# Kernel optimization log

Hardware: AMD Instinct MI355X
Metric: run time of the kernel (lower is better)

## Reference

```python
import jax, jax.numpy as jnp
import numpy as np

N = 1024
H = 4096
W = 4096
K_COUNTS = 10
IOU_T = 0.5
NEG = -1e30  # -inf stand-in for unrecorded groups


def _box_iou(b):
    # b: [N,4] xyxy pixel coords -> [N,N] IoU (torchvision.ops.box_iou)
    area = (b[:, 2] - b[:, 0]) * (b[:, 3] - b[:, 1])
    ix1 = jnp.maximum(b[:, None, 0], b[None, :, 0])
    iy1 = jnp.maximum(b[:, None, 1], b[None, :, 1])
    ix2 = jnp.minimum(b[:, None, 2], b[None, :, 2])
    iy2 = jnp.minimum(b[:, None, 3], b[None, :, 3])
    inter = jnp.clip(ix2 - ix1, 0.0) * jnp.clip(iy2 - iy1, 0.0)
    return inter / (area[:, None] + area[None, :] - inter)


def _c_wsl(iou_gt, scores, counts):
    # Faithful vectorized c_wsl_fast: for every start box i, greedily sweep
    # j = i+1..N-1 adding boxes compatible (IoU <= T) with all current members;
    # when a group hits `counts` at the TOP of a j-iteration it is recorded
    # (check-before-add semantics, so a group completed at j = N-1 is never
    # recorded, matching the original break-based control flow). The final
    # answer is the LAST start achieving the max recorded score (>= update).
    n = scores.shape[0]
    starts = jnp.arange(n)
    carry0 = (
        jnp.eye(n, dtype=bool),            # sel[i, k]: box k in group of start i
        jnp.ones(n, jnp.int32),            # group sizes
        scores,                            # group scores
        jnp.zeros(n, bool),                # recorded flag (== break)
        jnp.full(n, NEG, scores.dtype),    # recorded score
        jnp.zeros((n, n), bool),           # recorded membership
    )

    def step(c, xs):
        j, sj, iou_j = xs  # iou_j = iou_gt[j] (> T bool row; matrix symmetric)
        sel, size, score, rec, rec_score, rec_sel = c
        active = (j > starts) & (~rec)
        do_rec = active & (size == counts)
        rec_sel = jnp.where(do_rec[:, None], sel, rec_sel)
        rec_score = jnp.where(do_rec, score, rec_score)
        rec = rec | do_rec
        compat = ~jnp.any(sel & iou_j[None, :], axis=1)
        add = active & (~do_rec) & (size < counts) & compat
        sel = sel.at[:, j].set(sel[:, j] | add)
        size = size + add.astype(size.dtype)
        score = score + jnp.where(add, sj, jnp.zeros((), score.dtype))
        return (sel, size, score, rec, rec_score, rec_sel), None

    (_, _, _, rec, rec_score, rec_sel), _ = jax.lax.scan(
        step, carry0, (starts, scores, iou_gt))
    masked = jnp.where(rec, rec_score, NEG)
    best = (n - 1) - jnp.argmax(masked[::-1])  # last argmax == '>=' update rule
    return jnp.where(jnp.any(rec), rec_sel[best], jnp.zeros(n, bool))


def reference(bbox, obj_scores, probs, counts):
    Hh, Ww = probs.shape
    # score_bbox_heatmap(reduction='mean'): mean of probs[y1:y2, x1:x2] per box,
    # computed exactly for all boxes with a zero-padded summed-area table.
    sat = jnp.pad(jnp.cumsum(jnp.cumsum(probs, axis=0), axis=1), ((1, 0), (1, 0)))
    x1 = jnp.clip(jnp.floor(bbox[:, 0]).astype(jnp.int32), 0, Ww)
    y1 = jnp.clip(jnp.floor(bbox[:, 1]).astype(jnp.int32), 0, Hh)
    x2 = jnp.clip(jnp.floor(bbox[:, 2]).astype(jnp.int32), 0, Ww)
    y2 = jnp.clip(jnp.floor(bbox[:, 3]).astype(jnp.int32), 0, Hh)
    sums = sat[y2, x2] - sat[y1, x2] - sat[y2, x1] + sat[y1, x1]
    cnt = jnp.maximum((y2 - y1) * (x2 - x1), 1).astype(probs.dtype)
    box_scores = sums / cnt
    # agg_score_method == 'mean'
    scores = 0.5 * (obj_scores + box_scores)
    # sort descending, then greedy IoU grouping on sorted boxes
    order = jnp.argsort(-scores)
    bbox_s = bbox[order]
    scores_s = scores[order]
    iou_gt = _box_iou(bbox_s) > IOU_T
    sel = _c_wsl(iou_gt, scores_s, counts)
    return scores_s * sel.astype(scores_s.dtype)


def setup_inputs() -> dict:
    key = jax.random.key(0)
    k1, k2, k3, k4, k5, k6 = jax.random.split(key, 6)
    cx = jax.random.uniform(k1, (N,), minval=0.15, maxval=0.85) * W
    cy = jax.random.uniform(k2, (N,), minval=0.15, maxval=0.85) * H
    bw = jnp.maximum(jax.random.uniform(k3, (N,), minval=0.02, maxval=0.25) * W, 8.0)
    bh = jnp.maximum(jax.random.uniform(k4, (N,), minval=0.02, maxval=0.25) * H, 8.0)
    bbox = jnp.stack([cx - bw / 2, cy - bh / 2, cx + bw / 2, cy + bh / 2], axis=1)
    obj_scores = jax.random.uniform(k5, (N,))
    probs = jax.random.uniform(k6, (H, W))
    return {"bbox": bbox, "obj_scores": obj_scores, "probs": probs, "counts": K_COUNTS}
```

## Files before the change

kernel.cpp:

```cpp
#include <hip/hip_runtime.h>

#define HH 4096
#define WW 4096
#define NB 1024
#define NCHUNK 64
#define CROWS 64
#define IOU_T 0.5f

typedef unsigned long long u64;

constexpr size_t OFF_COORDS = 0;
constexpr size_t OFF_RD     = OFF_COORDS + (size_t)NB * 16;
constexpr size_t OFF_PART   = OFF_RD     + (size_t)HH * 16;
constexpr size_t OFF_SC64   = OFF_PART   + (size_t)NCHUNK * WW * 8;
constexpr size_t OFF_ORDER  = OFF_SC64   + (size_t)NB * 8;
constexpr size_t OFF_CTR    = OFF_ORDER  + (size_t)NB * 4;
constexpr size_t OFF_IOU    = OFF_CTR    + 64;
constexpr size_t OFF_RECSC  = OFF_IOU    + (size_t)NB * 16 * 8;
constexpr size_t OFF_RECSEL = OFF_RECSC  + (size_t)NB * 8;
constexpr size_t OFF_CC     = OFF_RECSEL + (size_t)NB * 16 * 8;


__global__ void __launch_bounds__(1024) k_setup(const float* __restrict__ bbox,
                        int4* coords, int4* rowdesc, int* ctr) {
    __shared__ int lf[HH];
    __shared__ int xlo[HH];
    __shared__ int xhi[HH];
    __shared__ int psum[256];
    int t = threadIdx.x;
    if (t == 0) *ctr = 0;
    for (int k = t; k < HH; k += 1024) { lf[k] = 0; xlo[k] = WW; xhi[k] = 0; }
    __syncthreads();
    if (t < NB) {
        int i = t;
        float b0 = bbox[i * 4 + 0], b1 = bbox[i * 4 + 1];
        float b2 = bbox[i * 4 + 2], b3 = bbox[i * 4 + 3];
        int x1 = min(max((int)floorf(b0), 0), WW);
        int y1 = min(max((int)floorf(b1), 0), HH);
        int x2 = min(max((int)floorf(b2), 0), WW);
        int y2 = min(max((int)floorf(b3), 0), HH);
        coords[i] = make_int4(x1, y1, x2, y2);
        if (y1 >= 1) {
            lf[y1 - 1] = 1;
            atomicMin(&xlo[y1 - 1], x1);
            atomicMax(&xhi[y1 - 1], x2);
        }
        if (y2 >= 1) {
            lf[y2 - 1] = 1;
            atomicMin(&xlo[y2 - 1], x1);
            atomicMax(&xhi[y2 - 1], x2);
        }
    }
    __syncthreads();
    if (t < 256) {
        int base = t * 16;
        int s = 0;
        for (int k = 0; k < 16; k++) s += lf[base + k];
        psum[t] = s;
    }
    __syncthreads();
    if (t < 64) {
        int v0 = psum[t * 4], v1 = psum[t * 4 + 1];
        int v2 = psum[t * 4 + 2], v3 = psum[t * 4 + 3];
        int lsum = v0 + v1 + v2 + v3;
        int incs = lsum;
        #pragma unroll
        for (int off = 1; off < 64; off <<= 1) {
            int n = __shfl_up(incs, off);
            if (t >= off) incs += n;
        }
        int ex = incs - lsum;
        psum[t * 4]     = ex;
        psum[t * 4 + 1] = ex + v0;
        psum[t * 4 + 2] = ex + v0 + v1;
        psum[t * 4 + 3] = ex + v0 + v1 + v2;
    }
    __syncthreads();
    if (t < 256) {
        int base = t * 16;
        int run = psum[t];
        for (int k = 0; k < 16; k++) {
            int r = base + k;
            int fl = lf[r];
            rowdesc[r] = make_int4(fl ? run : -1, xlo[r] >> 2, (xhi[r] + 3) >> 2, 0);
            run += fl;
        }
    }
}

__global__ void __launch_bounds__(256) k_stage(const float* __restrict__ probs,
        const int4* __restrict__ rowdesc,
        double* __restrict__ part, float* __restrict__ Cc) {
    __shared__ int4 rd_s[CROWS];
    int tid = blockIdx.x * 256 + threadIdx.x;
    int c  = tid >> 10;
    int xq = tid & 1023;
    if (threadIdx.x < CROWS) rd_s[threadIdx.x] = rowdesc[c * CROWS + threadIdx.x];
    __syncthreads();
    const float4* p = (const float4*)probs + (size_t)c * CROWS * (WW / 4) + xq;
    float4* Cc4 = (float4*)Cc;
    double a0 = 0.0, a1 = 0.0, a2 = 0.0, a3 = 0.0;
    for (int r = 0; r < CROWS; r += 8) {
        float4 q[8];
        #pragma unroll
        for (int k = 0; k < 8; k++) q[k] = p[(size_t)(r + k) * (WW / 4)];
        #pragma unroll
        for (int k = 0; k < 8; k++) {
            a0 += (double)q[k].x; a1 += (double)q[k].y;
            a2 += (double)q[k].z; a3 += (double)q[k].w;
            int4 d = rd_s[r + k];
            if (d.x >= 0 && xq >= d.y && xq < d.z)
                Cc4[(size_t)d.x * (WW / 4) + xq] =
                    make_float4((float)a0, (float)a1, (float)a2, (float)a3);
        }
    }
    double2* pp = (double2*)(part + (size_t)c * WW) + xq * 2;
    pp[0] = make_double2(a0, a1);
    pp[1] = make_double2(a2, a3);
}

__global__ void k_chunkscan(double* __restrict__ part) {
    int x = blockIdx.x * blockDim.x + threadIdx.x;
    double carry = 0.0;
    for (int g = 0; g < NCHUNK / 16; g++) {
        double v[16];
        #pragma unroll
        for (int k = 0; k < 16; k++) v[k] = part[(size_t)(g * 16 + k) * WW + x];
        #pragma unroll
        for (int k = 0; k < 16; k++) { double tv = v[k]; v[k] = carry; carry += tv; }
        #pragma unroll
        for (int k = 0; k < 16; k++) part[(size_t)(g * 16 + k) * WW + x] = v[k];
    }
}

__global__ void __launch_bounds__(64) k_boxsum(const int4* __restrict__ coords,
                         const float* __restrict__ obj,
                         const int4* __restrict__ rowdesc, const float* __restrict__ Cc,
                         const double* __restrict__ part,
                         double* sc64) {
    int i = blockIdx.x;
    int lane = threadIdx.x;
    int4 cd = coords[i];
    bool h1 = (cd.y >= 1), h2 = (cd.w >= 1);
    int s1 = h1 ? rowdesc[cd.y - 1].x : 0;
    int s2 = h2 ? rowdesc[cd.w - 1].x : 0;
    const float*  r2 = Cc   + (size_t)(h2 ? s2 : 0) * WW;
    const double* q2 = part + (size_t)(h2 ? ((cd.w - 1) >> 6) : 0) * WW;
    const float*  r1 = Cc   + (size_t)(h1 ? s1 : 0) * WW;
    const double* q1 = part + (size_t)(h1 ? ((cd.y - 1) >> 6) : 0) * WW;
    double s = 0.0;
    for (int x = cd.x + lane; x < cd.z; x += 64) {
        double v2 = h2 ? ((double)r2[x] + q2[x]) : 0.0;
        double v1 = h1 ? ((double)r1[x] + q1[x]) : 0.0;
        s += (v2 - v1);
    }
    #pragma unroll
    for (int off = 32; off > 0; off >>= 1) s += __shfl_down(s, off);
    if (lane == 0) {
        long long cnt = (long long)(cd.w - cd.y) * (long long)(cd.z - cd.x);
        if (cnt < 1) cnt = 1;
        double box = s / (double)cnt;
        sc64[i] = 0.5 * ((double)obj[i] + box);
    }
}

__global__ void __launch_bounds__(128) k_rank(const double* __restrict__ sc64,
                                              int* __restrict__ order) {
    __shared__ double s[NB];
    int t = threadIdx.x;
    for (int k = t; k < NB; k += 128) s[k] = sc64[k];
    __syncthreads();
    int i = blockIdx.x * 128 + t;
    double si = s[i];
    int rank = 0;
    #pragma unroll 8
    for (int j = 0; j < NB; j++) {
        double sj = s[j];
        rank += (sj > si) || (sj == si && j < i);
    }
    order[rank] = i;
}

__global__ void k_iou(const int* __restrict__ order, const float* __restrict__ bbox,
                      u64* __restrict__ ioub) {
    int tid = blockIdx.x * blockDim.x + threadIdx.x;
    int i = tid >> 10;
    int j = tid & (NB - 1);
    float4 a = ((const float4*)bbox)[order[i]];
    float4 b = ((const float4*)bbox)[order[j]];
    float ai = (a.z - a.x) * (a.w - a.y);
    float aj = (b.z - b.x) * (b.w - b.y);
    float ix1 = fmaxf(a.x, b.x), iy1 = fmaxf(a.y, b.y);
    float ix2 = fminf(a.z, b.z), iy2 = fminf(a.w, b.w);
    float iw = fmaxf(ix2 - ix1, 0.0f), ih = fmaxf(iy2 - iy1, 0.0f);
    float inter = iw * ih;
    float iou_v = inter / (ai + aj - inter);
    bool bit = iou_v > IOU_T;
    u64 m = __ballot(bit);
    if ((threadIdx.x & 63) == 0) ioub[(size_t)i * 16 + (j >> 6)] = m;
}

__global__ void __launch_bounds__(64) k_group(const u64* __restrict__ ioub,
                        const int* __restrict__ order,
                        const double* __restrict__ sc64,
                        const int* __restrict__ counts,
                        double* __restrict__ recsc,
                        u64* __restrict__ recsel,
                        int* __restrict__ ctr,
                        float* __restrict__ out) {
    __shared__ double ssd_s[NB];
    __shared__ int lastflag;
    int t = threadIdx.x;
    int i = blockIdx.x * 64 + t;
    for (int k = t; k < NB; k += 64) ssd_s[k] = sc64[order[k]];
    __syncthreads();
    int K = counts[0];
    u64 inc[16], sel[16];
    int wi = i >> 6, bi = i & 63;
    #pragma unroll
    for (int w = 0; w < 16; w++) {
        inc[w] = ioub[(size_t)i * 16 + w];
        sel[w] = (w == wi) ? (1ULL << bi) : 0ULL;
    }
    int size = 1;
    double score = ssd_s[i];
    int last = i;
    #pragma unroll
    for (int w = 0; w < 16; w++) {
        if (w < wi || size >= K) continue;
        u64 avail = ~inc[w];
        if (w == wi) avail &= (bi == 63) ? 0ULL : (~0ULL << (bi + 1));
        while (avail != 0ULL && size < K) {
            int b = __builtin_ctzll(avail);
            int j = (w << 6) + b;
            sel[w] |= 1ULL << b;
            size++;
            score += ssd_s[j];
            last = j;
            const u64* rj = ioub + (size_t)j * 16;
            #pragma unroll
            for (int w2 = 0; w2 < 16; w2++) inc[w2] |= rj[w2];
            avail &= ~inc[w];
            avail &= ~(1ULL << b);
        }
    }
    int rec = (size == K) && (last < NB - 1);
    recsc[i] = rec ? score : -1e300;
    #pragma unroll
    for (int w = 0; w < 16; w++) recsel[(size_t)i * 16 + w] = sel[w];
    __threadfence();
    if (t == 0) lastflag = (atomicAdd(ctr, 1) == (int)gridDim.x - 1);
    __syncthreads();
    if (!lastflag) return;
    __threadfence();
    double bs = -1e301; int bidx = 0;
    for (int m = 0; m < 16; m++) {
        int k = t * 16 + m;
        double v = recsc[k];
        if (v >= bs) { bs = v; bidx = k; }
    }
    #pragma unroll
    for (int off = 32; off > 0; off >>= 1) {
        double ob = __shfl_down(bs, off);
        int oi = __shfl_down(bidx, off);
        if (ob > bs || (ob == bs && oi > bidx)) { bs = ob; bidx = oi; }
    }
    bs = __shfl(bs, 0);
    bidx = __shfl(bidx, 0);
    int any = bs > -1e299;
    for (int k = t; k < NB; k += 64) {
        float v = 0.0f;
        if (any && ((recsel[(size_t)bidx * 16 + (k >> 6)] >> (k & 63)) & 1ULL))
            v = (float)ssd_s[k];
        out[k] = v;
    }
}


extern "C" void kernel_launch(void* const* d_in, const int* in_sizes, int n_in,
                              void* d_out, int out_size, void* d_ws, size_t ws_size,
                              hipStream_t stream) {
    const float* bbox  = (const float*)d_in[0];
    const float* obj   = (const float*)d_in[1];
    const float* probs = (const float*)d_in[2];
    const int*   counts = (const int*)d_in[3];
    float* out = (float*)d_out;

    char* w = (char*)d_ws;
    int4*   coords  = (int4*)(w + OFF_COORDS);
    int4*   rowdesc = (int4*)(w + OFF_RD);
    double* part    = (double*)(w + OFF_PART);
    double* sc64    = (double*)(w + OFF_SC64);
    int*    order   = (int*)(w + OFF_ORDER);
    int*    ctr     = (int*)(w + OFF_CTR);
    u64*    ioub    = (u64*)(w + OFF_IOU);
    double* recsc   = (double*)(w + OFF_RECSC);
    u64*    recsel  = (u64*)(w + OFF_RECSEL);
    float*  Cc      = (float*)(w + OFF_CC);

    k_setup<<<1, 1024, 0, stream>>>(bbox, coords, rowdesc, ctr);
    k_stage<<<(NCHUNK * WW / 4) / 256, 256, 0, stream>>>(probs, rowdesc, part, Cc);
    k_chunkscan<<<WW / 256, 256, 0, stream>>>(part);
    k_boxsum<<<NB, 64, 0, stream>>>(coords, obj, rowdesc, Cc, part, sc64);
    k_rank<<<NB / 128, 128, 0, stream>>>(sc64, order);
    k_iou<<<(NB * NB) / 256, 256, 0, stream>>>(order, bbox, ioub);
    k_group<<<NB / 64, 64, 0, stream>>>(ioub, order, sc64, counts, recsc, recsel,
                                        ctr, out);
}
```

Measured before the change: 179.7 us.

## Fold setup into stage kernel, use finer chunks and parallel chunk scan

```diff
diff --git a/kernel.cpp b/kernel.cpp
--- a/kernel.cpp
+++ b/kernel.cpp
@@ -3,15 +3,13 @@
 #define HH 4096
 #define WW 4096
 #define NB 1024
-#define NCHUNK 64
-#define CROWS 64
+#define NCHUNK 256
+#define CROWS 16
 #define IOU_T 0.5f
 
 typedef unsigned long long u64;
 
-constexpr size_t OFF_COORDS = 0;
-constexpr size_t OFF_RD     = OFF_COORDS + (size_t)NB * 16;
-constexpr size_t OFF_PART   = OFF_RD     + (size_t)HH * 16;
+constexpr size_t OFF_PART   = 0;
 constexpr size_t OFF_SC64   = OFF_PART   + (size_t)NCHUNK * WW * 8;
 constexpr size_t OFF_ORDER  = OFF_SC64   + (size_t)NB * 8;
 constexpr size_t OFF_CTR    = OFF_ORDER  + (size_t)NB * 4;
@@ -21,83 +19,35 @@
 constexpr size_t OFF_CC     = OFF_RECSEL + (size_t)NB * 16 * 8;
 
 
-__global__ void __launch_bounds__(1024) k_setup(const float* __restrict__ bbox,
-                        int4* coords, int4* rowdesc, int* ctr) {
-    __shared__ int lf[HH];
-    __shared__ int xlo[HH];
-    __shared__ int xhi[HH];
-    __shared__ int psum[256];
-    int t = threadIdx.x;
-    if (t == 0) *ctr = 0;
-    for (int k = t; k < HH; k += 1024) { lf[k] = 0; xlo[k] = WW; xhi[k] = 0; }
-    __syncthreads();
-    if (t < NB) {
-        int i = t;
-        float b0 = bbox[i * 4 + 0], b1 = bbox[i * 4 + 1];
-        float b2 = bbox[i * 4 + 2], b3 = bbox[i * 4 + 3];
-        int x1 = min(max((int)floorf(b0), 0), WW);
-        int y1 = min(max((int)floorf(b1), 0), HH);
-        int x2 = min(max((int)floorf(b2), 0), WW);
-        int y2 = min(max((int)floorf(b3), 0), HH);
-        coords[i] = make_int4(x1, y1, x2, y2);
-        if (y1 >= 1) {
-            lf[y1 - 1] = 1;
-            atomicMin(&xlo[y1 - 1], x1);
-            atomicMax(&xhi[y1 - 1], x2);
-        }
-        if (y2 >= 1) {
-            lf[y2 - 1] = 1;
-            atomicMin(&xlo[y2 - 1], x1);
-            atomicMax(&xhi[y2 - 1], x2);
-        }
-    }
-    __syncthreads();
-    if (t < 256) {
-        int base = t * 16;
-        int s = 0;
-        for (int k = 0; k < 16; k++) s += lf[base + k];
-        psum[t] = s;
-    }
-    __syncthreads();
-    if (t < 64) {
-        int v0 = psum[t * 4], v1 = psum[t * 4 + 1];
-        int v2 = psum[t * 4 + 2], v3 = psum[t * 4 + 3];
-        int lsum = v0 + v1 + v2 + v3;
-        int incs = lsum;
-        #pragma unroll
-        for (int off = 1; off < 64; off <<= 1) {
-            int n = __shfl_up(incs, off);
-            if (t >= off) incs += n;
-        }
-        int ex = incs - lsum;
-        psum[t * 4]     = ex;
-        psum[t * 4 + 1] = ex + v0;
-        psum[t * 4 + 2] = ex + v0 + v1;
-        psum[t * 4 + 3] = ex + v0 + v1 + v2;
-    }
-    __syncthreads();
-    if (t < 256) {
-        int base = t * 16;
-        int run = psum[t];
-        for (int k = 0; k < 16; k++) {
-            int r = base + k;
-            int fl = lf[r];
-            rowdesc[r] = make_int4(fl ? run : -1, xlo[r] >> 2, (xhi[r] + 3) >> 2, 0);
-            run += fl;
-        }
-    }
-}
-
 __global__ void __launch_bounds__(256) k_stage(const float* __restrict__ probs,
-        const int4* __restrict__ rowdesc,
+        const float* __restrict__ bbox,
         double* __restrict__ part, float* __restrict__ Cc) {
-    __shared__ int4 rd_s[CROWS];
+    __shared__ int xlo_s[CROWS], xhi_s[CROWS];
+    __shared__ int2 rng_s[CROWS];
     int tid = blockIdx.x * 256 + threadIdx.x;
     int c  = tid >> 10;
     int xq = tid & 1023;
-    if (threadIdx.x < CROWS) rd_s[threadIdx.x] = rowdesc[c * CROWS + threadIdx.x];
-    __syncthreads();
-    const float4* p = (const float4*)probs + (size_t)c * CROWS * (WW / 4) + xq;
+    int t  = threadIdx.x;
+    if (t < CROWS) { xlo_s[t] = WW + 1; xhi_s[t] = -1; }
+    __syncthreads();
+    int r0 = c * CROWS;
+    for (int i = t; i < NB; i += 256) {
+        float4 bb = ((const float4*)bbox)[i];
+        int x1 = min(max((int)floorf(bb.x), 0), WW);
+        int y1 = min(max((int)floorf(bb.y), 0), HH);
+        int x2 = min(max((int)floorf(bb.z), 0), WW);
+        int y2 = min(max((int)floorf(bb.w), 0), HH);
+        int ra = y1 - 1 - r0, rb = y2 - 1 - r0;
+        if (ra >= 0 && ra < CROWS) { atomicMin(&xlo_s[ra], x1); atomicMax(&xhi_s[ra], x2); }
+        if (rb >= 0 && rb < CROWS) { atomicMin(&xlo_s[rb], x1); atomicMax(&xhi_s[rb], x2); }
+    }
+    __syncthreads();
+    if (t < CROWS) {
+        int lo = xlo_s[t], hi = xhi_s[t];
+        rng_s[t] = (hi >= 0) ? make_int2(lo >> 2, (hi + 3) >> 2) : make_int2(1, 0);
+    }
+    __syncthreads();
+    const float4* p = (const float4*)probs + (size_t)r0 * (WW / 4) + xq;
     float4* Cc4 = (float4*)Cc;
     double a0 = 0.0, a1 = 0.0, a2 = 0.0, a3 = 0.0;
     for (int r = 0; r < CROWS; r += 8) {
@@ -108,9 +58,9 @@
         for (int k = 0; k < 8; k++) {
             a0 += (double)q[k].x; a1 += (double)q[k].y;
             a2 += (double)q[k].z; a3 += (double)q[k].w;
-            int4 d = rd_s[r + k];
-            if (d.x >= 0 && xq >= d.y && xq < d.z)
-                Cc4[(size_t)d.x * (WW / 4) + xq] =
+            int2 d = rng_s[r + k];
+            if (xq >= d.x && xq < d.y)
+                Cc4[(size_t)(r0 + r + k) * (WW / 4) + xq] =
                     make_float4((float)a0, (float)a1, (float)a2, (float)a3);
         }
     }
@@ -119,48 +69,60 @@
     pp[1] = make_double2(a2, a3);
 }
 
-__global__ void k_chunkscan(double* __restrict__ part) {
-    int x = blockIdx.x * blockDim.x + threadIdx.x;
-    double carry = 0.0;
-    for (int g = 0; g < NCHUNK / 16; g++) {
-        double v[16];
-        #pragma unroll
-        for (int k = 0; k < 16; k++) v[k] = part[(size_t)(g * 16 + k) * WW + x];
-        #pragma unroll
-        for (int k = 0; k < 16; k++) { double tv = v[k]; v[k] = carry; carry += tv; }
-        #pragma unroll
-        for (int k = 0; k < 16; k++) part[(size_t)(g * 16 + k) * WW + x] = v[k];
-    }
-}
-
-__global__ void __launch_bounds__(64) k_boxsum(const int4* __restrict__ coords,
+__global__ void __launch_bounds__(256) k_chunkscan(double* __restrict__ part,
+                                                   int* __restrict__ ctr) {
+    if (blockIdx.x == 0 && threadIdx.x == 0) *ctr = 0;
+    __shared__ double wsum[4];
+    int col = blockIdx.x;
+    int t = threadIdx.x;
+    int lane = t & 63, wv = t >> 6;
+    double v = part[(size_t)t * WW + col];
+    double inc = v;
+    #pragma unroll
+    for (int off = 1; off < 64; off <<= 1) {
+        double n = __shfl_up(inc, off);
+        if (lane >= off) inc += n;
+    }
+    if (lane == 63) wsum[wv] = inc;
+    __syncthreads();
+    double woff = 0.0;
+    for (int w = 0; w < 3; w++) if (w < wv) woff += wsum[w];
+    part[(size_t)t * WW + col] = woff + (inc - v);
+}
+
+__global__ void __launch_bounds__(256) k_boxsum(const float* __restrict__ bbox,
                          const float* __restrict__ obj,
-                         const int4* __restrict__ rowdesc, const float* __restrict__ Cc,
+                         const float* __restrict__ Cc,
                          const double* __restrict__ part,
-                         double* sc64) {
+                         double* __restrict__ sc64) {
     int i = blockIdx.x;
-    int lane = threadIdx.x;
-    int4 cd = coords[i];
-    bool h1 = (cd.y >= 1), h2 = (cd.w >= 1);
-    int s1 = h1 ? rowdesc[cd.y - 1].x : 0;
-    int s2 = h2 ? rowdesc[cd.w - 1].x : 0;
-    const float*  r2 = Cc   + (size_t)(h2 ? s2 : 0) * WW;
-    const double* q2 = part + (size_t)(h2 ? ((cd.w - 1) >> 6) : 0) * WW;
-    const float*  r1 = Cc   + (size_t)(h1 ? s1 : 0) * WW;
-    const double* q1 = part + (size_t)(h1 ? ((cd.y - 1) >> 6) : 0) * WW;
+    int t = threadIdx.x;
+    float4 bb = ((const float4*)bbox)[i];
+    int x1 = min(max((int)floorf(bb.x), 0), WW);
+    int y1 = min(max((int)floorf(bb.y), 0), HH);
+    int x2 = min(max((int)floorf(bb.z), 0), WW);
+    int y2 = min(max((int)floorf(bb.w), 0), HH);
+    bool h1 = (y1 >= 1), h2 = (y2 >= 1);
+    const float*  r2 = Cc   + (size_t)(h2 ? (y2 - 1) : 0) * WW;
+    const double* q2 = part + (size_t)(h2 ? ((y2 - 1) >> 4) : 0) * WW;
+    const float*  r1 = Cc   + (size_t)(h1 ? (y1 - 1) : 0) * WW;
+    const double* q1 = part + (size_t)(h1 ? ((y1 - 1) >> 4) : 0) * WW;
     double s = 0.0;
-    for (int x = cd.x + lane; x < cd.z; x += 64) {
+    for (int x = x1 + t; x < x2; x += 256) {
         double v2 = h2 ? ((double)r2[x] + q2[x]) : 0.0;
         double v1 = h1 ? ((double)r1[x] + q1[x]) : 0.0;
         s += (v2 - v1);
     }
+    __shared__ double red[4];
     #pragma unroll
     for (int off = 32; off > 0; off >>= 1) s += __shfl_down(s, off);
-    if (lane == 0) {
-        long long cnt = (long long)(cd.w - cd.y) * (long long)(cd.z - cd.x);
+    if ((t & 63) == 0) red[t >> 6] = s;
+    __syncthreads();
+    if (t == 0) {
+        double tot = red[0] + red[1] + red[2] + red[3];
+        long long cnt = (long long)(y2 - y1) * (long long)(x2 - x1);
         if (cnt < 1) cnt = 1;
-        double box = s / (double)cnt;
-        sc64[i] = 0.5 * ((double)obj[i] + box);
+        sc64[i] = 0.5 * ((double)obj[i] + tot / (double)cnt);
     }
 }
 
@@ -287,8 +249,6 @@
     float* out = (float*)d_out;
 
     char* w = (char*)d_ws;
-    int4*   coords  = (int4*)(w + OFF_COORDS);
-    int4*   rowdesc = (int4*)(w + OFF_RD);
     double* part    = (double*)(w + OFF_PART);
     double* sc64    = (double*)(w + OFF_SC64);
     int*    order   = (int*)(w + OFF_ORDER);
@@ -298,10 +258,9 @@
     u64*    recsel  = (u64*)(w + OFF_RECSEL);
     float*  Cc      = (float*)(w + OFF_CC);
 
-    k_setup<<<1, 1024, 0, stream>>>(bbox, coords, rowdesc, ctr);
-    k_stage<<<(NCHUNK * WW / 4) / 256, 256, 0, stream>>>(probs, rowdesc, part, Cc);
-    k_chunkscan<<<WW / 256, 256, 0, stream>>>(part);
-    k_boxsum<<<NB, 64, 0, stream>>>(coords, obj, rowdesc, Cc, part, sc64);
+    k_stage<<<(NCHUNK * WW / 4) / 256, 256, 0, stream>>>(probs, bbox, part, Cc);
+    k_chunkscan<<<WW, 256, 0, stream>>>(part, ctr);
+    k_boxsum<<<NB, 256, 0, stream>>>(bbox, obj, Cc, part, sc64);
     k_rank<<<NB / 128, 128, 0, stream>>>(sc64, order);
     k_iou<<<(NB * NB) / 256, 256, 0, stream>>>(order, bbox, ioub);
     k_group<<<NB / 64, 64, 0, stream>>>(ioub, order, sc64, counts, recsc, recsel,
```

After: 186.2 us. +3.6%, slower.
